# Kernel optimization log

Hardware: AMD Instinct MI355X
Metric: run time of the kernel (lower is better)

The kernel has to match this reference:

```python
import jax, jax.numpy as jnp
import numpy as np

NUM_HEADS = 32
MICRO_BATCHES = 2
TOP_K = 2
LN_EPS = 1e-5


def _mha(x, scale, bias, wq, wk, wv, wo):
    # Pre-LN multi-head self-attention with residual (RealSelfAttention).
    B, S, D = x.shape
    H = NUM_HEADS
    hd = D // H
    res = x
    mu = jnp.mean(x, axis=-1, keepdims=True)
    xc = x - mu
    var = jnp.mean(xc * xc, axis=-1, keepdims=True)
    xn = xc / jnp.sqrt(var + LN_EPS) * scale + bias
    q = (xn @ wq.T).reshape(B, S, H, hd).transpose(0, 2, 1, 3)
    k = (xn @ wk.T).reshape(B, S, H, hd).transpose(0, 2, 1, 3)
    v = (xn @ wv.T).reshape(B, S, H, hd).transpose(0, 2, 1, 3)
    scores = jnp.einsum('bhqd,bhkd->bhqk', q, k) * (1.0 / np.sqrt(hd).astype(np.float32))
    attn = jax.nn.softmax(scores, axis=-1)
    o = jnp.einsum('bhqk,bhkd->bhqd', attn, v).transpose(0, 2, 1, 3).reshape(B, S, D)
    return o @ wo.T + res


def setup_inputs() -> dict:
    key = jax.random.key(0)
    D, E, F = 1024, 8, 4096
    B, S = 4, 1024
    ks = jax.random.split(key, 16)
    w = lambda k, shape: (jax.random.normal(k, shape, dtype=jnp.float32) * 0.02)
    return {
        'x': jax.random.normal(ks[0], (B, S, D), dtype=jnp.float32),
        'ln1_scale': jnp.ones((D,), jnp.float32),
        'ln1_bias': jnp.zeros((D,), jnp.float32),
        'wq1': w(ks[1], (D, D)), 'wk1': w(ks[2], (D, D)),
        'wv1': w(ks[3], (D, D)), 'wo1': w(ks[4], (D, D)),
        'gate_w': w(ks[5], (E, D)),
        'exp_w1': w(ks[6], (E, F, D)), 'exp_b1': jnp.zeros((E, F), jnp.float32),
        'exp_w2': w(ks[7], (E, D, F)), 'exp_b2': jnp.zeros((E, D), jnp.float32),
        'ln2_scale': jnp.ones((D,), jnp.float32),
        'ln2_bias': jnp.zeros((D,), jnp.float32),
        'wq2': w(ks[8], (D, D)), 'wk2': w(ks[9], (D, D)),
        'wv2': w(ks[10], (D, D)), 'wo2': w(ks[11], (D, D)),
    }


def reference(x, ln1_scale, ln1_bias, wq1, wk1, wv1, wo1, gate_w,
              exp_w1, exp_b1, exp_w2, exp_b2,
              ln2_scale, ln2_bias, wq2, wk2, wv2, wo2):
    B, S, D = x.shape
    E = exp_w1.shape[0]
    # PreOps: attention layer L (per-sample, so full-batch apply == per-microbatch apply)
    y = _mha(x, ln1_scale, ln1_bias, wq1, wk1, wv1, wo1)
    # Gate: logits + top-k indices computed in source but never applied to tokens.
    flat = y.reshape(B * S, D)
    logits = flat @ gate_w.T
    _ = jax.lax.top_k(logits, TOP_K)  # indices unused downstream (faithful to source)
    # Dispatch (all_to_all on 1 device == identity): per-microbatch flat tokens are
    # chunked equally across local experts.
    T = (B // MICRO_BATCHES) * S            # tokens per microbatch
    toks = y.reshape(MICRO_BATCHES, E, T // E, D)
    h = jax.nn.gelu(jnp.einsum('metd,efd->metf', toks, exp_w1) + exp_b1[None, :, None, :],
                    approximate=False)
    eo = jnp.einsum('metf,edf->metd', h, exp_w2) + exp_b2[None, :, None, :]
    # Combine (identity) + PostOps: attention layer L+1
    z = eo.reshape(B, S, D)
    out = _mha(z, ln2_scale, ln2_bias, wq2, wk2, wv2, wo2)
    return out
```

## Files before the change

kernel.cpp:

```cpp
#include <hip/hip_runtime.h>
#include <hip/hip_bf16.h>

typedef __attribute__((ext_vector_type(8))) short bf16x8;
typedef __attribute__((ext_vector_type(4))) float f32x4;
typedef __attribute__((ext_vector_type(4))) short short4v;

#define DEV __device__ __forceinline__

DEV short f2bf(float f) {
  union { float f; unsigned u; } x; x.f = f;
  unsigned r = x.u + 0x7fffu + ((x.u >> 16) & 1u);
  return (short)(r >> 16);
}

DEV short f2bf_hw(float f) {
  union { __hip_bfloat16 h; short s; } c;
  c.h = __float2bfloat16(f);
  return c.s;
}

DEV bf16x8 cvt8(f32x4 a, f32x4 b) {
  union { short s[8]; bf16x8 v; } o;
  o.s[0] = f2bf_hw(a[0]); o.s[1] = f2bf_hw(a[1]);
  o.s[2] = f2bf_hw(a[2]); o.s[3] = f2bf_hw(a[3]);
  o.s[4] = f2bf_hw(b[0]); o.s[5] = f2bf_hw(b[1]);
  o.s[6] = f2bf_hw(b[2]); o.s[7] = f2bf_hw(b[3]);
  return o.v;
}

template <int N> DEV void vmwait() {
  if constexpr (N == 0) asm volatile("s_waitcnt vmcnt(0)" ::: "memory");
  else if constexpr (N == 3) asm volatile("s_waitcnt vmcnt(3)" ::: "memory");
  else if constexpr (N == 4) asm volatile("s_waitcnt vmcnt(4)" ::: "memory");
  else if constexpr (N == 6) asm volatile("s_waitcnt vmcnt(6)" ::: "memory");
}

#define GL2LDS16(g, l) __builtin_amdgcn_global_load_lds(                      \
    (const __attribute__((address_space(1))) void*)(g),                       \
    (__attribute__((address_space(3))) void*)(l), 16, 0, 0)

__global__ __launch_bounds__(256) void k_cast_bf16(const float* __restrict__ s,
                                                   short* __restrict__ d, int n4) {
  int i = blockIdx.x * 256 + threadIdx.x;
  if (i >= n4) return;
  float4 v = ((const float4*)s)[i];
  short4v o;
  o[0] = f2bf(v.x); o[1] = f2bf(v.y); o[2] = f2bf(v.z); o[3] = f2bf(v.w);
  ((short4v*)d)[i] = o;
}

__global__ __launch_bounds__(256)
void k_ln(const float* __restrict__ X, const float* __restrict__ G,
          const float* __restrict__ Bi, short* __restrict__ Y) {
  const int row = blockIdx.x, t = threadIdx.x;
  const float4 v = ((const float4*)(X + (size_t)row * 1024))[t];
  float s = v.x + v.y + v.z + v.w;
  float s2 = v.x * v.x + v.y * v.y + v.z * v.z + v.w * v.w;
#pragma unroll
  for (int m = 1; m < 64; m <<= 1) { s += __shfl_xor(s, m); s2 += __shfl_xor(s2, m); }
  __shared__ float rs[4], rq[4];
  const int w = t >> 6, lane = t & 63;
  if (lane == 0) { rs[w] = s; rq[w] = s2; }
  __syncthreads();
  s = rs[0] + rs[1] + rs[2] + rs[3];
  s2 = rq[0] + rq[1] + rq[2] + rq[3];
  const float mu = s * (1.f / 1024.f);
  const float var = s2 * (1.f / 1024.f) - mu * mu;
  const float rstd = rsqrtf(var + 1e-5f);
  const float4 g = ((const float4*)G)[t];
  const float4 bi = ((const float4*)Bi)[t];
  short4v o;
  o[0] = f2bf((v.x - mu) * rstd * g.x + bi.x);
  o[1] = f2bf((v.y - mu) * rstd * g.y + bi.y);
  o[2] = f2bf((v.z - mu) * rstd * g.z + bi.z);
  o[3] = f2bf((v.w - mu) * rstd * g.w + bi.w);
  ((short4v*)(Y + (size_t)row * 1024))[t] = o;
}

template <int EPI, int EXPERT, int BN, int BF32>
__global__ __launch_bounds__(256)
void k_gemm_bt(const short* __restrict__ A, const void* __restrict__ Btv,
               void* __restrict__ Cv, const float* __restrict__ Res,
               const float* __restrict__ Bias, int M, int N, int K, int xt) {
  constexpr int NF = BN / 32;
  constexpr int BR = BN / 64;
  constexpr int LOADS = 2 + (BF32 ? NF : BR);
  __shared__ __attribute__((aligned(16))) short As[3][128 * 32];
  __shared__ __attribute__((aligned(16))) char Braw[3][BN * 32 * (BF32 ? 4 : 2)];
  const int tid = threadIdx.x;
  const int w = tid >> 6, lane = tid & 63;
  const int r16 = lane & 15, kg = lane >> 4;
  const int wr = w >> 1, wc = w & 1;

  const int bid = blockIdx.x;
  int bx;
  size_t rowBase, bOff = 0, biasOff = 0;
  if constexpr (EXPERT) {
    int e = bid & 7, mb = (bid >> 3) & 1, by = (bid >> 4) & 1;
    bx = bid >> 5;
    rowBase = (size_t)by * 128 + (size_t)(mb * 8 + e) * 256;
    bOff = (size_t)e * N * K;
    biasOff = (size_t)e * N;
  } else {
    int y7 = bid & 7, r = bid >> 3;
    bx = r % xt;
    rowBase = (size_t)(y7 + 8 * (r / xt)) * 128;
  }
  const size_t col0 = (size_t)bx * BN;
  const short* Ab = A + rowBase * K;
  const short* Bb16 = (const short*)Btv + bOff + col0 * K;
  const float* Bb32 = (const float*)Btv + bOff + col0 * K;

  f32x4 acc[4][NF] = {};

  auto stage = [&](int buf, int k0) {
#pragma unroll
    for (int i = 0; i < 2; ++i) {
      int c = (i * 4 + w) * 64 + lane;
      int row = c >> 2;
      int sl = (c & 3) ^ (row & 3);
      GL2LDS16(Ab + (size_t)row * K + k0 + sl * 8, (char*)As[buf] + (size_t)(i * 4 + w) * 1024);
    }
    if constexpr (BF32) {
#pragma unroll
      for (int i = 0; i < NF; ++i) {
        int c = i * 256 + tid;
        int row = c >> 3;
        int sl = (c & 7) ^ (row & 7);
        GL2LDS16(Bb32 + (size_t)row * K + k0 + sl * 4, (char*)Braw[buf] + (size_t)(i * 4 + w) * 1024);
      }
    } else {
#pragma unroll
      for (int i = 0; i < BR; ++i) {
        int c = i * 256 + tid;
        int row = c >> 2;
        int sl = (c & 3) ^ (row & 3);
        GL2LDS16(Bb16 + (size_t)row * K + k0 + sl * 8, (char*)Braw[buf] + (size_t)(i * 4 + w) * 1024);
      }
    }
  };

  stage(0, 0);
  stage(1, 32);
  vmwait<LOADS>();
  __builtin_amdgcn_s_barrier();

  int cur = 0;
  for (int k0 = 0; k0 < K; k0 += 32) {
    int cn = cur + 1; if (cn == 3) cn = 0;
    int c2 = cn + 1; if (c2 == 3) c2 = 0;
    const bool more = (k0 + 64 < K);
    if (more) stage(c2, k0 + 64);

    bf16x8 af[4], bg[NF];
#pragma unroll
    for (int m = 0; m < 4; ++m) {
      int row = wr * 64 + m * 16 + r16;
      af[m] = *(const bf16x8*)(As[cur] + row * 32 + (kg ^ (row & 3)) * 8);
    }
    if constexpr (BF32) {
      const float* Bf = (const float*)Braw[cur];
#pragma unroll
      for (int n = 0; n < NF; ++n) {
        int row = wc * (BN / 2) + n * 16 + r16;
        int s0 = (2 * kg) ^ (row & 7), s1 = (2 * kg + 1) ^ (row & 7);
        f32x4 fa = *(const f32x4*)(Bf + row * 32 + s0 * 4);
        f32x4 fb = *(const f32x4*)(Bf + row * 32 + s1 * 4);
        bg[n] = cvt8(fa, fb);
      }
    } else {
      const short* Bh = (const short*)Braw[cur];
#pragma unroll
      for (int n = 0; n < NF; ++n) {
        int row = wc * (BN / 2) + n * 16 + r16;
        bg[n] = *(const bf16x8*)(Bh + row * 32 + (kg ^ (row & 3)) * 8);
      }
    }
#pragma unroll
    for (int m = 0; m < 4; ++m)
#pragma unroll
      for (int n = 0; n < NF; ++n)
        acc[m][n] = __builtin_amdgcn_mfma_f32_16x16x32_bf16(af[m], bg[n], acc[m][n], 0, 0, 0);

    if (more) vmwait<LOADS>(); else vmwait<0>();
    __builtin_amdgcn_s_barrier();
    cur = cn;
  }

#pragma unroll
  for (int m = 0; m < 4; ++m) {
    size_t grow0 = rowBase + wr * 64 + m * 16 + kg * 4;
#pragma unroll
    for (int n = 0; n < NF; ++n) {
      size_t gcol = col0 + wc * (BN / 2) + n * 16 + r16;
#pragma unroll
      for (int r = 0; r < 4; ++r) {
        size_t idx = (grow0 + r) * (size_t)N + gcol;
        float v = acc[m][n][r];
        if constexpr (EPI == 1 || EPI == 4) v += Res[idx];
        if constexpr (EPI == 2 || EPI == 3) v += Bias[biasOff + gcol];
        if constexpr (EPI == 2) v = 0.5f * v * (1.f + erff(v * 0.70710678118654752f));
        if constexpr (EPI <= 2) ((short*)Cv)[idx] = f2bf(v);
        else                    ((float*)Cv)[idx] = v;
      }
    }
  }
  (void)M;
}

__global__ __launch_bounds__(256, 3)
void k_attn(const short* __restrict__ QKV, short* __restrict__ O) {
  const int bid = blockIdx.x;
  const int qt = bid >> 7, h = bid & 31, b = (bid >> 5) & 3;
  const int tid = threadIdx.x, w = tid >> 6, lane = tid & 63;
  const int r16 = lane & 15, kg = lane >> 4;

  __shared__ __attribute__((aligned(16))) short Kl[2][128 * 32];
  __shared__ __attribute__((aligned(16))) short Vt[2][32 * 128];
  __shared__ __attribute__((aligned(16))) short Pl[4][16 * 128];

  const size_t tb = (size_t)b * 1024;
  const int qbase = qt * 128 + w * 32;

  bf16x8 aq[2];
#pragma unroll
  for (int f = 0; f < 2; ++f)
    aq[f] = *(const bf16x8*)(QKV + (tb + qbase + f * 16 + r16) * 3072 + h * 32 + kg * 8);

  f32x4 acc[2][2] = {};
  float lreg[2][4] = {};
  const float scale = 0.17677669529663687f;

  auto stageK = [&](int bid2, int kc) {
#pragma unroll
    for (int i = 0; i < 2; ++i) {
      int c = (i * 4 + w) * 64 + lane;
      int row = c >> 2;
      int sl = (c & 3) ^ (row & 3);
      GL2LDS16(QKV + (tb + kc * 128 + row) * 3072 + 1024 + h * 32 + sl * 8,
               (char*)Kl[bid2] + (size_t)(i * 4 + w) * 1024);
    }
  };

  stageK(0, 0);
  {
    int c0 = tid,        vr0 = c0 >> 2, d00 = (c0 & 3) * 8;
    int c1 = 256 + tid,  vr1 = c1 >> 2, d01 = (c1 & 3) * 8;
    bf16x8 v0 = *(const bf16x8*)(QKV + (tb + vr0) * 3072 + 2048 + h * 32 + d00);
    bf16x8 v1 = *(const bf16x8*)(QKV + (tb + vr1) * 3072 + 2048 + h * 32 + d01);
#pragma unroll
    for (int j = 0; j < 8; ++j) {
      int da = d00 + j, db = d01 + j;
      Vt[0][((da * 128 + vr0) ^ ((da & 7) << 3))] = v0[j];
      Vt[0][((db * 128 + vr1) ^ ((db & 7) << 3))] = v1[j];
    }
  }
  __syncthreads();

  int bi = 0;
  for (int kc = 0; kc < 8; ++kc) {
    bf16x8 nv0, nv1;
    int nvr0 = 0, nd0 = 0, nvr1 = 0, nd1 = 0;
    if (kc < 7) {
      stageK(bi ^ 1, kc + 1);
      const short* Vg = QKV + (tb + (size_t)(kc + 1) * 128) * 3072 + 2048 + h * 32;
      int c0 = tid;       nvr0 = c0 >> 2; nd0 = (c0 & 3) * 8;
      int c1 = 256 + tid; nvr1 = c1 >> 2; nd1 = (c1 & 3) * 8;
      nv0 = *(const bf16x8*)(Vg + (size_t)nvr0 * 3072 + nd0);
      nv1 = *(const bf16x8*)(Vg + (size_t)nvr1 * 3072 + nd1);
    }

    f32x4 s[2][8];
#pragma unroll
    for (int kt = 0; kt < 8; ++kt) {
      int row = kt * 16 + r16;
      bf16x8 bk = *(const bf16x8*)(Kl[bi] + row * 32 + (kg ^ (row & 3)) * 8);
      f32x4 zz = {0.f, 0.f, 0.f, 0.f};
      s[0][kt] = __builtin_amdgcn_mfma_f32_16x16x32_bf16(aq[0], bk, zz, 0, 0, 0);
      s[1][kt] = __builtin_amdgcn_mfma_f32_16x16x32_bf16(aq[1], bk, zz, 0, 0, 0);
    }

#pragma unroll
    for (int f = 0; f < 2; ++f)
#pragma unroll
      for (int r = 0; r < 4; ++r) {
        float sum = 0.f;
#pragma unroll
        for (int kt = 0; kt < 8; ++kt) {
          float p = __expf(s[f][kt][r] * scale);
          s[f][kt][r] = p;
          sum += p;
        }
#pragma unroll
        for (int m = 1; m < 16; m <<= 1) sum += __shfl_xor(sum, m);
        lreg[f][r] += sum;
      }

    short* P = Pl[w];
#pragma unroll
    for (int f = 0; f < 2; ++f) {
#pragma unroll
      for (int kt = 0; kt < 8; ++kt)
#pragma unroll
        for (int r = 0; r < 4; ++r) {
          int row = kg * 4 + r;
          P[((row * 128 + kt * 16 + r16) ^ ((row & 7) << 3))] = f2bf(s[f][kt][r]);
        }
#pragma unroll
      for (int ks = 0; ks < 4; ++ks) {
        bf16x8 pa = *(const bf16x8*)(P + ((r16 * 128 + ks * 32 + kg * 8) ^ ((r16 & 7) << 3)));
#pragma unroll
        for (int dt = 0; dt < 2; ++dt) {
          int vrow = dt * 16 + r16;
          bf16x8 bv = *(const bf16x8*)(Vt[bi] + ((vrow * 128 + ks * 32 + kg * 8) ^ ((vrow & 7) << 3)));
          acc[f][dt] = __builtin_amdgcn_mfma_f32_16x16x32_bf16(pa, bv, acc[f][dt], 0, 0, 0);
        }
      }
    }

    if (kc < 7) {
#pragma unroll
      for (int j = 0; j < 8; ++j) {
        int da = nd0 + j, db = nd1 + j;
        Vt[bi ^ 1][((da * 128 + nvr0) ^ ((da & 7) << 3))] = nv0[j];
        Vt[bi ^ 1][((db * 128 + nvr1) ^ ((db & 7) << 3))] = nv1[j];
      }
    }

    __syncthreads();
    bi ^= 1;
  }

#pragma unroll
  for (int f = 0; f < 2; ++f)
#pragma unroll
    for (int r = 0; r < 4; ++r) {
      float inv = 1.f / lreg[f][r];
      size_t qrow = tb + qbase + f * 16 + kg * 4 + r;
#pragma unroll
      for (int dt = 0; dt < 2; ++dt)
        O[qrow * 1024 + h * 32 + dt * 16 + r16] = f2bf(acc[f][dt][r] * inv);
    }
}

extern "C" void kernel_launch(void* const* d_in, const int* in_sizes, int n_in,
                              void* d_out, int out_size, void* d_ws, size_t ws_size,
                              hipStream_t stream) {
  const float* x    = (const float*)d_in[0];
  const float* ln1s = (const float*)d_in[1];
  const float* ln1b = (const float*)d_in[2];
  const float* wq1  = (const float*)d_in[3];
  const float* wk1  = (const float*)d_in[4];
  const float* wv1  = (const float*)d_in[5];
  const float* wo1  = (const float*)d_in[6];
  const float* ew1  = (const float*)d_in[8];
  const float* eb1  = (const float*)d_in[9];
  const float* ew2  = (const float*)d_in[10];
  const float* eb2  = (const float*)d_in[11];
  const float* ln2s = (const float*)d_in[12];
  const float* ln2b = (const float*)d_in[13];
  const float* wq2  = (const float*)d_in[14];
  const float* wk2  = (const float*)d_in[15];
  const float* wv2  = (const float*)d_in[16];
  const float* wo2  = (const float*)d_in[17];

  char* ws = (char*)d_ws;
  size_t off = 0;
  auto alloc = [&](size_t bytes) {
    char* p = ws + off;
    off += (bytes + 255) & ~(size_t)255;
    return p;
  };
  short* wqkv1b = (short*)alloc(3072ull * 1024 * 2);
  short* wo1b   = (short*)alloc(1024ull * 1024 * 2);
  short* wqkv2b = (short*)alloc(3072ull * 1024 * 2);
  short* wo2b   = (short*)alloc(1024ull * 1024 * 2);
  short* xnb    = (short*)alloc(4096ull * 1024 * 2);
  short* qkvo   = (short*)alloc(4096ull * 4096 * 2);
  short* ybf    = (short*)alloc(4096ull * 1024 * 2);
  float* zf     = (float*)alloc(4096ull * 1024 * 4);
  (void)ws_size; (void)in_sizes; (void)n_in; (void)out_size;

  short* QKV = qkvo;
  short* Ob  = qkvo + 4096ull * 3072;
  short* hb  = qkvo;

  auto cast = [&](const float* s, short* d, size_t n) {
    int n4 = (int)(n / 4);
    k_cast_bf16<<<(n4 + 255) / 256, 256, 0, stream>>>(s, d, n4);
  };
  cast(wq1, wqkv1b,           1048576);
  cast(wk1, wqkv1b + 1048576, 1048576);
  cast(wv1, wqkv1b + 2097152, 1048576);
  cast(wo1, wo1b,             1048576);
  cast(wq2, wqkv2b,           1048576);
  cast(wk2, wqkv2b + 1048576, 1048576);
  cast(wv2, wqkv2b + 2097152, 1048576);
  cast(wo2, wo2b,             1048576);

  k_ln<<<4096, 256, 0, stream>>>(x, ln1s, ln1b, xnb);
  k_gemm_bt<0, 0, 128, 0><<<768, 256, 0, stream>>>(xnb, wqkv1b, QKV, nullptr, nullptr, 4096, 3072, 1024, 24);
  k_attn<<<1024, 256, 0, stream>>>(QKV, Ob);
  k_gemm_bt<1, 0, 64, 0><<<512, 256, 0, stream>>>(Ob, wo1b, ybf, x, nullptr, 4096, 1024, 1024, 16);
  k_gemm_bt<2, 1, 128, 1><<<1024, 256, 0, stream>>>(ybf, ew1, hb, nullptr, eb1, 256, 4096, 1024, 0);
  k_gemm_bt<3, 1, 64, 1><<<512, 256, 0, stream>>>(hb, ew2, zf, nullptr, eb2, 256, 1024, 4096, 0);
  k_ln<<<4096, 256, 0, stream>>>(zf, ln2s, ln2b, xnb);
  k_gemm_bt<0, 0, 128, 0><<<768, 256, 0, stream>>>(xnb, wqkv2b, QKV, nullptr, nullptr, 4096, 3072, 1024, 24);
  k_attn<<<1024, 256, 0, stream>>>(QKV, Ob);
  k_gemm_bt<4, 0, 64, 0><<<512, 256, 0, stream>>>(Ob, wo2b, (float*)d_out, zf, nullptr, 4096, 1024, 1024, 16);
}
```

Measured before the change: 541.1 us.

## Merge weight casts into two launches, use hardware bf16 convert, defer softmax sum reduction

Replaces eight per-matrix cast launches with two 2D-grid launches that each convert four contiguous weight matrices. All float-to-bf16 conversions switch from a software round-to-nearest-even routine to the hardware bf16 intrinsic. In attention, the cross-lane shuffle reduction of the softmax denominator moves out of the key loop and runs once at the end. Relies on wo buffers sitting contiguously after the qkv buffers in the workspace.

Result: slower. 608.6 us (+12.5%).

```diff
diff --git a/kernel.cpp b/kernel.cpp
--- a/kernel.cpp
+++ b/kernel.cpp
@@ -6,12 +6,6 @@
 typedef __attribute__((ext_vector_type(4))) short short4v;
 
 #define DEV __device__ __forceinline__
-
-DEV short f2bf(float f) {
-  union { float f; unsigned u; } x; x.f = f;
-  unsigned r = x.u + 0x7fffu + ((x.u >> 16) & 1u);
-  return (short)(r >> 16);
-}
 
 DEV short f2bf_hw(float f) {
   union { __hip_bfloat16 h; short s; } c;
@@ -39,14 +33,17 @@
     (const __attribute__((address_space(1))) void*)(g),                       \
     (__attribute__((address_space(3))) void*)(l), 16, 0, 0)
 
-__global__ __launch_bounds__(256) void k_cast_bf16(const float* __restrict__ s,
-                                                   short* __restrict__ d, int n4) {
+__global__ __launch_bounds__(256)
+void k_cast4(const float* __restrict__ s0, const float* __restrict__ s1,
+             const float* __restrict__ s2, const float* __restrict__ s3,
+             short* __restrict__ d) {
+  const int which = blockIdx.y;
+  const float* s = which == 0 ? s0 : which == 1 ? s1 : which == 2 ? s2 : s3;
   int i = blockIdx.x * 256 + threadIdx.x;
-  if (i >= n4) return;
   float4 v = ((const float4*)s)[i];
   short4v o;
-  o[0] = f2bf(v.x); o[1] = f2bf(v.y); o[2] = f2bf(v.z); o[3] = f2bf(v.w);
-  ((short4v*)d)[i] = o;
+  o[0] = f2bf_hw(v.x); o[1] = f2bf_hw(v.y); o[2] = f2bf_hw(v.z); o[3] = f2bf_hw(v.w);
+  ((short4v*)(d + (size_t)which * 1048576))[i] = o;
 }
 
 __global__ __launch_bounds__(256)
@@ -70,10 +67,10 @@
   const float4 g = ((const float4*)G)[t];
   const float4 bi = ((const float4*)Bi)[t];
   short4v o;
-  o[0] = f2bf((v.x - mu) * rstd * g.x + bi.x);
-  o[1] = f2bf((v.y - mu) * rstd * g.y + bi.y);
-  o[2] = f2bf((v.z - mu) * rstd * g.z + bi.z);
-  o[3] = f2bf((v.w - mu) * rstd * g.w + bi.w);
+  o[0] = f2bf_hw((v.x - mu) * rstd * g.x + bi.x);
+  o[1] = f2bf_hw((v.y - mu) * rstd * g.y + bi.y);
+  o[2] = f2bf_hw((v.z - mu) * rstd * g.z + bi.z);
+  o[3] = f2bf_hw((v.w - mu) * rstd * g.w + bi.w);
   ((short4v*)(Y + (size_t)row * 1024))[t] = o;
 }
 
@@ -200,7 +197,7 @@
         if constexpr (EPI == 1 || EPI == 4) v += Res[idx];
         if constexpr (EPI == 2 || EPI == 3) v += Bias[biasOff + gcol];
         if constexpr (EPI == 2) v = 0.5f * v * (1.f + erff(v * 0.70710678118654752f));
-        if constexpr (EPI <= 2) ((short*)Cv)[idx] = f2bf(v);
+        if constexpr (EPI <= 2) ((short*)Cv)[idx] = f2bf_hw(v);
         else                    ((float*)Cv)[idx] = v;
       }
     }
@@ -228,7 +225,7 @@
     aq[f] = *(const bf16x8*)(QKV + (tb + qbase + f * 16 + r16) * 3072 + h * 32 + kg * 8);
 
   f32x4 acc[2][2] = {};
-  float lreg[2][4] = {};
+  float lsum[2][4] = {};
   const float scale = 0.17677669529663687f;
 
   auto stageK = [&](int bid2, int kc) {
@@ -291,9 +288,7 @@
           s[f][kt][r] = p;
           sum += p;
         }
-#pragma unroll
-        for (int m = 1; m < 16; m <<= 1) sum += __shfl_xor(sum, m);
-        lreg[f][r] += sum;
+        lsum[f][r] += sum;
       }
 
     short* P = Pl[w];
@@ -304,7 +299,7 @@
 #pragma unroll
         for (int r = 0; r < 4; ++r) {
           int row = kg * 4 + r;
-          P[((row * 128 + kt * 16 + r16) ^ ((row & 7) << 3))] = f2bf(s[f][kt][r]);
+          P[((row * 128 + kt * 16 + r16) ^ ((row & 7) << 3))] = f2bf_hw(s[f][kt][r]);
         }
 #pragma unroll
       for (int ks = 0; ks < 4; ++ks) {
@@ -335,11 +330,14 @@
   for (int f = 0; f < 2; ++f)
 #pragma unroll
     for (int r = 0; r < 4; ++r) {
-      float inv = 1.f / lreg[f][r];
+      float sum = lsum[f][r];
+#pragma unroll
+      for (int m = 1; m < 16; m <<= 1) sum += __shfl_xor(sum, m);
+      float inv = 1.f / sum;
       size_t qrow = tb + qbase + f * 16 + kg * 4 + r;
 #pragma unroll
       for (int dt = 0; dt < 2; ++dt)
-        O[qrow * 1024 + h * 32 + dt * 16 + r16] = f2bf(acc[f][dt][r] * inv);
+        O[qrow * 1024 + h * 32 + dt * 16 + r16] = f2bf_hw(acc[f][dt][r] * inv);
     }
 }
 
@@ -384,28 +382,19 @@
   short* QKV = qkvo;
   short* Ob  = qkvo + 4096ull * 3072;
   short* hb  = qkvo;
-
-  auto cast = [&](const float* s, short* d, size_t n) {
-    int n4 = (int)(n / 4);
-    k_cast_bf16<<<(n4 + 255) / 256, 256, 0, stream>>>(s, d, n4);
-  };
-  cast(wq1, wqkv1b,           1048576);
-  cast(wk1, wqkv1b + 1048576, 1048576);
-  cast(wv1, wqkv1b + 2097152, 1048576);
-  cast(wo1, wo1b,             1048576);
-  cast(wq2, wqkv2b,           1048576);
-  cast(wk2, wqkv2b + 1048576, 1048576);
-  cast(wv2, wqkv2b + 2097152, 1048576);
-  cast(wo2, wo2b,             1048576);
+  (void)wo1b; (void)wo2b;
+
+  k_cast4<<<dim3(1024, 4), 256, 0, stream>>>(wq1, wk1, wv1, wo1, wqkv1b);
+  k_cast4<<<dim3(1024, 4), 256, 0, stream>>>(wq2, wk2, wv2, wo2, wqkv2b);
 
   k_ln<<<4096, 256, 0, stream>>>(x, ln1s, ln1b, xnb);
   k_gemm_bt<0, 0, 128, 0><<<768, 256, 0, stream>>>(xnb, wqkv1b, QKV, nullptr, nullptr, 4096, 3072, 1024, 24);
   k_attn<<<1024, 256, 0, stream>>>(QKV, Ob);
-  k_gemm_bt<1, 0, 64, 0><<<512, 256, 0, stream>>>(Ob, wo1b, ybf, x, nullptr, 4096, 1024, 1024, 16);
+  k_gemm_bt<1, 0, 64, 0><<<512, 256, 0, stream>>>(Ob, wqkv1b + 3145728, ybf, x, nullptr, 4096, 1024, 1024, 16);
   k_gemm_bt<2, 1, 128, 1><<<1024, 256, 0, stream>>>(ybf, ew1, hb, nullptr, eb1, 256, 4096, 1024, 0);
   k_gemm_bt<3, 1, 64, 1><<<512, 256, 0, stream>>>(hb, ew2, zf, nullptr, eb2, 256, 1024, 4096, 0);
   k_ln<<<4096, 256, 0, stream>>>(zf, ln2s, ln2b, xnb);
   k_gemm_bt<0, 0, 128, 0><<<768, 256, 0, stream>>>(xnb, wqkv2b, QKV, nullptr, nullptr, 4096, 3072, 1024, 24);
   k_attn<<<1024, 256, 0, stream>>>(QKV, Ob);
-  k_gemm_bt<4, 0, 64, 0><<<512, 256, 0, stream>>>(Ob, wo2b, (float*)d_out, zf, nullptr, 4096, 1024, 1024, 16);
-}
+  k_gemm_bt<4, 0, 64, 0><<<512, 256, 0, stream>>>(Ob, wqkv2b + 3145728, (float*)d_out, zf, nullptr, 4096, 1024, 1024, 16);
+}
```
